# Kernel optimization log

Measured on AMD Instinct MI355X. Metric: run time of the kernel, lower is better.

Reference implementation:

```python
import jax, jax.numpy as jnp
import numpy as np

NUM_HEADS = 8
EMBED_CH = 512   # k channels
OUT_CH = 256     # v channels
MASK_CURRENT = False
NEG_INF = -1e30


def setup_inputs() -> dict:
    key = jax.random.key(0)
    ks = jax.random.split(key, 7)
    N, C, H, W = 8, 256, 32, 32
    s = lambda fan: 1.0 / np.sqrt(fan)
    return {
        "x": jax.random.normal(ks[0], (N, C, H, W), jnp.float32),
        "Wq": jax.random.normal(ks[1], (EMBED_CH, C), jnp.float32) * s(C),
        "bq": jax.random.normal(ks[2], (EMBED_CH,), jnp.float32) * 0.01,
        "Wkv": jax.random.normal(ks[3], (EMBED_CH + OUT_CH, C), jnp.float32) * s(C),
        "bkv": jax.random.normal(ks[4], (EMBED_CH + OUT_CH,), jnp.float32) * 0.01,
        "Wo": jax.random.normal(ks[5], (OUT_CH, OUT_CH), jnp.float32) * s(OUT_CH),
        "bo": jax.random.normal(ks[6], (OUT_CH,), jnp.float32) * 0.01,
    }


def _to_multihead(t, n, T):
    # t: [n, h*d, T] with channel layout '(h d)' -> [n, h, T, d]
    h = NUM_HEADS
    return t.reshape(n, h, -1, T).transpose(0, 1, 3, 2)


def reference(x, Wq, bq, Wkv, bkv, Wo, bo):
    n, C, H, W = x.shape
    T = H * W
    xf = x.reshape(n, C, T)  # flatten spatial dims into sequence

    # 1x1 convs == pointwise channel GEMMs
    q = jnp.einsum('oc,nct->not', Wq, xf) + bq[None, :, None]
    kv = jnp.einsum('oc,nct->not', Wkv, xf) + bkv[None, :, None]
    k, v = kv[:, :EMBED_CH], kv[:, EMBED_CH:]

    q = _to_multihead(q, n, T)   # [n, h, T, dk]
    k = _to_multihead(k, n, T)   # [n, h, T, dk]
    v = _to_multihead(v, n, T)   # [n, h, T, dv]

    dk = k.shape[-1]
    scale = 1.0 / np.sqrt(dk).astype(np.float32)

    # causal mask over flattened spatial positions (lower-triangular)
    diag = -1 if MASK_CURRENT else 0
    mask = jnp.tril(jnp.ones((T, T), dtype=bool), k=diag)  # [T, T]

    attn = jnp.einsum('nhtd,nhsd->nhts', q, k) * scale
    attn = jnp.where(mask[None, None], attn, NEG_INF)
    attn = jax.nn.softmax(attn, axis=-1)
    attn = jnp.where(mask[None, None], attn, 0.0)

    out = jnp.einsum('nhts,nhsd->nhtd', attn, v)            # [n, h, T, dv]
    out = out.transpose(0, 1, 3, 2).reshape(n, OUT_CH, T)   # n (h d) t

    out = jnp.einsum('oc,nct->not', Wo, out) + bo[None, :, None]
    return out.reshape(n, OUT_CH, H, W)
```

## Files before the change

### kernel.cpp

```cpp
#include <hip/hip_runtime.h>
#include <hip/hip_bf16.h>
#include <math.h>

typedef __bf16 bf16;
typedef __attribute__((ext_vector_type(4))) __bf16 bf16x4;
typedef __attribute__((ext_vector_type(8))) __bf16 bf16x8;
typedef __attribute__((ext_vector_type(4))) float f32x4;

#define T_DIM 1024
#define C_DIM 256
#define HEADS 8

static __device__ __forceinline__ int tb(int row, int col) {
  return row * 128 + ((((col >> 3) ^ row) & 7) << 4) + ((col & 7) << 1);
}

static __device__ __forceinline__ void gl16(const char* g, char* l) {
  __builtin_amdgcn_global_load_lds(
      (const __attribute__((address_space(1))) unsigned int*)g,
      (__attribute__((address_space(3))) unsigned int*)l, 16, 0, 0);
}
static __device__ __forceinline__ void stage16k(const char* g, char* l, int tid) {
  const int w = (tid >> 6) * 1024, ln = (tid & 63) * 16;
#pragma unroll
  for (int i = 0; i < 4; ++i) gl16(g + i * 4096 + w + ln, l + i * 4096 + w);
}
static __device__ __forceinline__ void stage8k(const char* g, char* l, int tid) {
  const int w = (tid >> 6) * 1024, ln = (tid & 63) * 16;
#pragma unroll
  for (int i = 0; i < 2; ++i) gl16(g + i * 4096 + w + ln, l + i * 4096 + w);
}
static __device__ __forceinline__ void stage4k(const char* g, char* l, int tid) {
  gl16(g + (tid >> 6) * 1024 + (tid & 63) * 16, l + (tid >> 6) * 1024);
}

__global__ __launch_bounds__(256) void k_prep(const float* __restrict__ x,
    const float* __restrict__ Wq, const float* __restrict__ Wkv, const float* __restrict__ Wo,
    char* __restrict__ xTt, char* __restrict__ Wbt, char* __restrict__ Wot) {
  const int tid = threadIdx.x;
  const int b = blockIdx.x;
  if (b < 512) {
    __shared__ float tile[64][65];
    const int n = b >> 6, rem = b & 63, tt64 = rem >> 2, ct = (rem & 3) << 6;
    const float* xp = x + ((size_t)n * C_DIM + ct) * T_DIM + tt64 * 64;
    const int t = tid & 63, c0 = tid >> 6;
#pragma unroll
    for (int i = 0; i < 16; ++i) tile[c0 + i * 4][t] = xp[(size_t)(c0 + i * 4) * T_DIM + t];
    __syncthreads();
    char* dst = xTt + (((size_t)(n * 8 + (tt64 >> 1))) * 4 + (rem & 3)) * 16384;
    const int rbase = (tt64 & 1) * 64;
#pragma unroll
    for (int i = 0; i < 2; ++i) {
      const int idx = tid + i * 256;
      const int tl = idx >> 3, c8 = (idx & 7) * 8;
      bf16x8 v;
#pragma unroll
      for (int j = 0; j < 8; ++j) v[j] = (bf16)tile[c8 + j][tl];
      *(bf16x8*)(dst + tb(rbase + tl, c8)) = v;
    }
  } else {
    const bool isWo = (b >= 532);
    const int o0 = (b - (isWo ? 532 : 512)) * 64;
#pragma unroll
    for (int i = 0; i < 8; ++i) {
      const int idx = tid + i * 256;
      const int row = idx >> 5, c8 = (idx & 31) * 8;
      const int o = o0 + row;
      const float* src = isWo ? (Wo + (size_t)o * C_DIM + c8)
                              : (o < 512 ? Wq + (size_t)o * C_DIM + c8
                                         : Wkv + (size_t)(o - 512) * C_DIM + c8);
      float4 a = *(const float4*)src;
      float4 bq4 = *(const float4*)(src + 4);
      bf16x8 v;
      v[0]=(bf16)a.x; v[1]=(bf16)a.y; v[2]=(bf16)a.z; v[3]=(bf16)a.w;
      v[4]=(bf16)bq4.x; v[5]=(bf16)bq4.y; v[6]=(bf16)bq4.z; v[7]=(bf16)bq4.w;
      char* base = isWo ? Wot : Wbt;
      char* dst = base + (((size_t)(o >> 7)) * 4 + (c8 >> 6)) * 16384;
      *(bf16x8*)(dst + tb(o & 127, c8 & 63)) = v;
    }
  }
}

__global__ __launch_bounds__(256) void k_qkv(const char* __restrict__ Wbt, const char* __restrict__ xTt,
    const float* __restrict__ bq, const float* __restrict__ bkv,
    bf16* __restrict__ q_ws, char* __restrict__ Kt, char* __restrict__ Vt) {
  __shared__ __attribute__((aligned(128))) unsigned char smem[32768];
  const int tid = threadIdx.x;
  const int nt = blockIdx.x, mt = blockIdx.y, n = blockIdx.z;
  const int w = tid >> 6, lane = tid & 63, lrow = lane & 15, lg = lane >> 4;
  const int wm = (w >> 1) * 64, wn = (w & 1) * 64;
  const char* gA = Wbt + (size_t)mt * 65536;
  const char* gB = xTt + ((size_t)(n * 8 + nt)) * 65536;

  f32x4 acc[4][4] = {};
#pragma unroll 1
  for (int kk = 0; kk < 4; ++kk) {
    stage16k(gA + kk * 16384, (char*)smem, tid);
    stage16k(gB + kk * 16384, (char*)smem + 16384, tid);
    __syncthreads();
    const char* As = (const char*)smem;
    const char* Bs = As + 16384;
    bf16x8 af[4][2], bv[4][2];
#pragma unroll
    for (int mi = 0; mi < 4; ++mi)
#pragma unroll
      for (int kh = 0; kh < 2; ++kh)
        af[mi][kh] = *(const bf16x8*)(As + tb(wm + mi * 16 + lrow, kh * 32 + lg * 8));
#pragma unroll
    for (int ni = 0; ni < 4; ++ni)
#pragma unroll
      for (int kh = 0; kh < 2; ++kh)
        bv[ni][kh] = *(const bf16x8*)(Bs + tb(wn + ni * 16 + lrow, kh * 32 + lg * 8));
#pragma unroll
    for (int kh = 0; kh < 2; ++kh)
#pragma unroll
      for (int mi = 0; mi < 4; ++mi)
#pragma unroll
        for (int ni = 0; ni < 4; ++ni)
          acc[mi][ni] = __builtin_amdgcn_mfma_f32_16x16x32_bf16(af[mi][kh], bv[ni][kh], acc[mi][ni], 0, 0, 0);
    __syncthreads();
  }

  const int obase = mt * 128 + wm + lg * 4;
  const int tcol0 = nt * 128 + wn + lrow;
#pragma unroll
  for (int mi = 0; mi < 4; ++mi) {
    const int o = obase + mi * 16;
    if (mt < 4) {
      const float4 bb = *(const float4*)(bq + o);
      const int nh = n * 8 + (o >> 6), d = o & 63;
      bf16* qrow = q_ws + (size_t)nh * (T_DIM * 64) + d;
#pragma unroll
      for (int ni = 0; ni < 4; ++ni) {
        const int t = tcol0 + ni * 16;
        f32x4 v = acc[mi][ni];
        bf16x4 pk;
        pk[0]=(bf16)(v[0]+bb.x); pk[1]=(bf16)(v[1]+bb.y); pk[2]=(bf16)(v[2]+bb.z); pk[3]=(bf16)(v[3]+bb.w);
        *(bf16x4*)(qrow + (size_t)t * 64) = pk;
      }
    } else if (mt < 8) {
      const int o2 = o - 512;
      const float4 bb = *(const float4*)(bkv + o2);
      const int nh = n * 8 + (o2 >> 6), d = o2 & 63;
      char* tbase = Kt + (size_t)nh * 16 * 8192;
#pragma unroll
      for (int ni = 0; ni < 4; ++ni) {
        const int t = tcol0 + ni * 16;
        f32x4 v = acc[mi][ni];
        bf16x4 pk;
        pk[0]=(bf16)(v[0]+bb.x); pk[1]=(bf16)(v[1]+bb.y); pk[2]=(bf16)(v[2]+bb.z); pk[3]=(bf16)(v[3]+bb.w);
        *(bf16x4*)(tbase + (t >> 6) * 8192 + tb(t & 63, d)) = pk;
      }
    } else {
      const int o3 = o - 1024;
      const float4 bb = *(const float4*)(bkv + 512 + o3);
      const float* bbp = (const float*)&bb;
      const int nh = n * 8 + (o3 >> 5), dv = o3 & 31;
      char* tbase = Vt + (size_t)nh * 16 * 4096;
#pragma unroll
      for (int ni = 0; ni < 4; ++ni) {
        const int t = tcol0 + ni * 16;
        f32x4 v = acc[mi][ni];
        char* tile = tbase + (t >> 6) * 4096;
#pragma unroll
        for (int r = 0; r < 4; ++r)
          *(bf16*)(tile + tb(dv + r, t & 63)) = (bf16)(v[r] + bbp[r]);
      }
    }
  }
}

__global__ __launch_bounds__(256) void k_attn(const bf16* __restrict__ q_ws,
    const char* __restrict__ Kt, const char* __restrict__ Vt, char* __restrict__ attTt) {
  __shared__ __attribute__((aligned(128))) unsigned char smem[20480];
  const int tid = threadIdx.x;
  const int nh = blockIdx.x, qp = blockIdx.y;
  const int w = tid >> 6, lane = tid & 63, lrow = lane & 15, lg = lane >> 4;

  const char* Ktb = Kt + (size_t)nh * 16 * 8192;
  const char* Vtb = Vt + (size_t)nh * 16 * 4096;
  const char* Kb = (const char*)smem;
  const char* Vb = (const char*)smem + 8192;
  char* pw = (char*)smem + 12288 + w * 2048;
  const int n = nh >> 3, h = nh & 7;
  const float s2 = 0.18033688f;

#pragma unroll 1
  for (int ph = 0; ph < 2; ++ph) {
    const int qt = ph ? (15 - qp) : qp;
    const int tg = qt * 64 + w * 16 + lrow;
    const bf16* qbase = q_ws + ((size_t)nh * T_DIM + tg) * 64;
    const bf16x8 qf0 = *(const bf16x8*)(qbase + lg * 8);
    const bf16x8 qf1 = *(const bf16x8*)(qbase + 32 + lg * 8);

    float m = -INFINITY, l = 0.f;
    f32x4 oacc[2] = {};

    for (int st = 0; st <= qt; ++st) {
      stage8k(Ktb + st * 8192, (char*)smem, tid);
      stage4k(Vtb + st * 4096, (char*)smem + 8192, tid);
      __syncthreads();

      f32x4 sacc[4];
#pragma unroll
      for (int rt = 0; rt < 4; ++rt) {
        f32x4 a = {0.f, 0.f, 0.f, 0.f};
        bf16x8 kf0 = *(const bf16x8*)(Kb + tb(rt * 16 + lrow, lg * 8));
        a = __builtin_amdgcn_mfma_f32_16x16x32_bf16(kf0, qf0, a, 0, 0, 0);
        bf16x8 kf1 = *(const bf16x8*)(Kb + tb(rt * 16 + lrow, 32 + lg * 8));
        a = __builtin_amdgcn_mfma_f32_16x16x32_bf16(kf1, qf1, a, 0, 0, 0);
        sacc[rt] = a;
      }

      float p[16];
      const bool diag = (st == qt);
      const int tl = w * 16 + lrow;
#pragma unroll
      for (int rt = 0; rt < 4; ++rt)
#pragma unroll
        for (int r = 0; r < 4; ++r) {
          float v = sacc[rt][r] * s2;
          if (diag && (rt * 16 + lg * 4 + r) > tl) v = -INFINITY;
          p[rt * 4 + r] = v;
        }

      float pmax = p[0];
#pragma unroll
      for (int i = 1; i < 16; ++i) pmax = fmaxf(pmax, p[i]);
      pmax = fmaxf(pmax, __shfl_xor(pmax, 16));
      pmax = fmaxf(pmax, __shfl_xor(pmax, 32));
      const float mn = fmaxf(m, pmax);
      const float corr = exp2f(m - mn);
      float ps = 0.f;
#pragma unroll
      for (int i = 0; i < 16; ++i) { p[i] = exp2f(p[i] - mn); ps += p[i]; }
      ps += __shfl_xor(ps, 16);
      ps += __shfl_xor(ps, 32);
      l = l * corr + ps;
      m = mn;
      oacc[0] = oacc[0] * corr;
      oacc[1] = oacc[1] * corr;

#pragma unroll
      for (int rt = 0; rt < 4; ++rt) {
        bf16x4 pk;
#pragma unroll
        for (int r = 0; r < 4; ++r) pk[r] = (bf16)p[rt * 4 + r];
        *(bf16x4*)(pw + tb(lrow, rt * 16 + lg * 4)) = pk;
      }

#pragma unroll
      for (int ks = 0; ks < 2; ++ks) {
        bf16x8 pf = *(const bf16x8*)(pw + tb(lrow, ks * 32 + lg * 8));
#pragma unroll
        for (int dt = 0; dt < 2; ++dt) {
          bf16x8 vf = *(const bf16x8*)(Vb + tb(dt * 16 + lrow, ks * 32 + lg * 8));
          oacc[dt] = __builtin_amdgcn_mfma_f32_16x16x32_bf16(vf, pf, oacc[dt], 0, 0, 0);
        }
      }
      __syncthreads();
    }

    const float inv = 1.0f / l;
    const int ntt = tg >> 7, row = tg & 127;
#pragma unroll
    for (int dt = 0; dt < 2; ++dt) {
      const int c = h * 32 + dt * 16 + lg * 4;
      char* tile = attTt + (((size_t)(n * 8 + ntt)) * 4 + (c >> 6)) * 16384;
      bf16x4 pk;
#pragma unroll
      for (int r = 0; r < 4; ++r) pk[r] = (bf16)(oacc[dt][r] * inv);
      *(bf16x4*)(tile + tb(row, c & 63)) = pk;
    }
  }
}

__global__ __launch_bounds__(256) void k_proj(const char* __restrict__ attTt,
    const char* __restrict__ Wot, const float* __restrict__ bo, float* __restrict__ out) {
  __shared__ __attribute__((aligned(128))) unsigned char smem[24576];
  const int tid = threadIdx.x;
  const int tm = blockIdx.x, om = blockIdx.y, n = blockIdx.z;
  const int w = tid >> 6, lane = tid & 63, lrow = lane & 15, lg = lane >> 4;
  const int wm = (w >> 1) * 64, wn = (w & 1) * 32;
  const char* gA = attTt + ((size_t)(n * 8 + tm)) * 65536;
  const char* gB = Wot + (size_t)(om >> 1) * 65536 + (om & 1) * 8192;

  f32x4 acc[4][2] = {};
#pragma unroll 1
  for (int kk = 0; kk < 4; ++kk) {
    stage16k(gA + kk * 16384, (char*)smem, tid);
    stage8k(gB + kk * 16384, (char*)smem + 16384, tid);
    __syncthreads();
    const char* As = (const char*)smem;
    const char* Bs = As + 16384;
    bf16x8 af[4][2], bv[2][2];
#pragma unroll
    for (int mi = 0; mi < 4; ++mi)
#pragma unroll
      for (int kh = 0; kh < 2; ++kh)
        af[mi][kh] = *(const bf16x8*)(As + tb(wm + mi * 16 + lrow, kh * 32 + lg * 8));
#pragma unroll
    for (int ni = 0; ni < 2; ++ni)
#pragma unroll
      for (int kh = 0; kh < 2; ++kh)
        bv[ni][kh] = *(const bf16x8*)(Bs + tb(wn + ni * 16 + lrow, kh * 32 + lg * 8));
#pragma unroll
    for (int kh = 0; kh < 2; ++kh)
#pragma unroll
      for (int mi = 0; mi < 4; ++mi)
#pragma unroll
        for (int ni = 0; ni < 2; ++ni)
          acc[mi][ni] = __builtin_amdgcn_mfma_f32_16x16x32_bf16(af[mi][kh], bv[ni][kh], acc[mi][ni], 0, 0, 0);
    __syncthreads();
  }

  const int t0b = tm * 128 + wm + lg * 4;
  const int ob = om * 64 + wn + lrow;
#pragma unroll
  for (int mi = 0; mi < 4; ++mi) {
    const int t0 = t0b + mi * 16;
#pragma unroll
    for (int ni = 0; ni < 2; ++ni) {
      const int o = ob + ni * 16;
      const float bb = bo[o];
      f32x4 v = acc[mi][ni];
      v[0] += bb; v[1] += bb; v[2] += bb; v[3] += bb;
      *(f32x4*)(out + ((size_t)(n * C_DIM + o)) * T_DIM + t0) = v;
    }
  }
}

extern "C" void kernel_launch(void* const* d_in, const int* in_sizes, int n_in,
                              void* d_out, int out_size, void* d_ws, size_t ws_size,
                              hipStream_t stream) {
  const float* x   = (const float*)d_in[0];
  const float* Wq  = (const float*)d_in[1];
  const float* bq  = (const float*)d_in[2];
  const float* Wkv = (const float*)d_in[3];
  const float* bkv = (const float*)d_in[4];
  const float* Wo  = (const float*)d_in[5];
  const float* bo  = (const float*)d_in[6];
  float* out = (float*)d_out;

  char* ws = (char*)d_ws;
  char* xTt   = ws;
  char* Wbt   = ws + (4u  << 20);
  char* Wot   = ws + (5u  << 20);
  bf16* q_ws  = (bf16*)(ws + (6u << 20));
  char* Kt    = ws + (14u << 20);
  char* Vt    = ws + (22u << 20);
  char* attTt = ws + (26u << 20);

  k_prep<<<536, 256, 0, stream>>>(x, Wq, Wkv, Wo, xTt, Wbt, Wot);
  k_qkv<<<dim3(8, 10, 8), 256, 0, stream>>>(Wbt, xTt, bq, bkv, q_ws, Kt, Vt);
  k_attn<<<dim3(64, 8), 256, 0, stream>>>(q_ws, Kt, Vt, attTt);
  k_proj<<<dim3(8, 4, 8), 256, 0, stream>>>(attTt, Wot, bo, out);
}
```

Before: 60.59 us.

## Process two KV tiles per attention iteration and stage V epilogue through LDS

```diff
diff --git a/kernel.cpp b/kernel.cpp
--- a/kernel.cpp
+++ b/kernel.cpp
@@ -84,7 +84,7 @@
 __global__ __launch_bounds__(256) void k_qkv(const char* __restrict__ Wbt, const char* __restrict__ xTt,
     const float* __restrict__ bq, const float* __restrict__ bkv,
     bf16* __restrict__ q_ws, char* __restrict__ Kt, char* __restrict__ Vt) {
-  __shared__ __attribute__((aligned(128))) unsigned char smem[32768];
+  __shared__ __attribute__((aligned(128))) unsigned char smem[34816];
   const int tid = threadIdx.x;
   const int nt = blockIdx.x, mt = blockIdx.y, n = blockIdx.z;
   const int w = tid >> 6, lane = tid & 63, lrow = lane & 15, lg = lane >> 4;
@@ -123,72 +123,92 @@
 
   const int obase = mt * 128 + wm + lg * 4;
   const int tcol0 = nt * 128 + wn + lrow;
-#pragma unroll
-  for (int mi = 0; mi < 4; ++mi) {
-    const int o = obase + mi * 16;
-    if (mt < 4) {
-      const float4 bb = *(const float4*)(bq + o);
-      const int nh = n * 8 + (o >> 6), d = o & 63;
-      bf16* qrow = q_ws + (size_t)nh * (T_DIM * 64) + d;
+  if (mt < 8) {
+#pragma unroll
+    for (int mi = 0; mi < 4; ++mi) {
+      const int o = obase + mi * 16;
+      if (mt < 4) {
+        const float4 bb = *(const float4*)(bq + o);
+        const int nh = n * 8 + (o >> 6), d = o & 63;
+        bf16* qrow = q_ws + (size_t)nh * (T_DIM * 64) + d;
+#pragma unroll
+        for (int ni = 0; ni < 4; ++ni) {
+          const int t = tcol0 + ni * 16;
+          f32x4 v = acc[mi][ni];
+          bf16x4 pk;
+          pk[0]=(bf16)(v[0]+bb.x); pk[1]=(bf16)(v[1]+bb.y); pk[2]=(bf16)(v[2]+bb.z); pk[3]=(bf16)(v[3]+bb.w);
+          *(bf16x4*)(qrow + (size_t)t * 64) = pk;
+        }
+      } else {
+        const int o2 = o - 512;
+        const float4 bb = *(const float4*)(bkv + o2);
+        const int nh = n * 8 + (o2 >> 6), d = o2 & 63;
+        char* tbase = Kt + (size_t)nh * 16 * 8192;
+#pragma unroll
+        for (int ni = 0; ni < 4; ++ni) {
+          const int t = tcol0 + ni * 16;
+          f32x4 v = acc[mi][ni];
+          bf16x4 pk;
+          pk[0]=(bf16)(v[0]+bb.x); pk[1]=(bf16)(v[1]+bb.y); pk[2]=(bf16)(v[2]+bb.z); pk[3]=(bf16)(v[3]+bb.w);
+          *(bf16x4*)(tbase + (t >> 6) * 8192 + tb(t & 63, d)) = pk;
+        }
+      }
+    }
+  } else {
+    bf16* tp = (bf16*)smem;
+#pragma unroll
+    for (int mi = 0; mi < 4; ++mi) {
+      const int o3g = (mt - 8) * 128 + wm + mi * 16 + lg * 4;
+      const float4 bb = *(const float4*)(bkv + 512 + o3g);
+      const float* bbp = (const float*)&bb;
+      const int o3l = wm + mi * 16 + lg * 4;
 #pragma unroll
       for (int ni = 0; ni < 4; ++ni) {
-        const int t = tcol0 + ni * 16;
+        const int tl = wn + ni * 16 + lrow;
         f32x4 v = acc[mi][ni];
-        bf16x4 pk;
-        pk[0]=(bf16)(v[0]+bb.x); pk[1]=(bf16)(v[1]+bb.y); pk[2]=(bf16)(v[2]+bb.z); pk[3]=(bf16)(v[3]+bb.w);
-        *(bf16x4*)(qrow + (size_t)t * 64) = pk;
-      }
-    } else if (mt < 8) {
-      const int o2 = o - 512;
-      const float4 bb = *(const float4*)(bkv + o2);
-      const int nh = n * 8 + (o2 >> 6), d = o2 & 63;
-      char* tbase = Kt + (size_t)nh * 16 * 8192;
-#pragma unroll
-      for (int ni = 0; ni < 4; ++ni) {
-        const int t = tcol0 + ni * 16;
-        f32x4 v = acc[mi][ni];
-        bf16x4 pk;
-        pk[0]=(bf16)(v[0]+bb.x); pk[1]=(bf16)(v[1]+bb.y); pk[2]=(bf16)(v[2]+bb.z); pk[3]=(bf16)(v[3]+bb.w);
-        *(bf16x4*)(tbase + (t >> 6) * 8192 + tb(t & 63, d)) = pk;
-      }
-    } else {
-      const int o3 = o - 1024;
-      const float4 bb = *(const float4*)(bkv + 512 + o3);
-      const float* bbp = (const float*)&bb;
-      const int nh = n * 8 + (o3 >> 5), dv = o3 & 31;
-      char* tbase = Vt + (size_t)nh * 16 * 4096;
-#pragma unroll
-      for (int ni = 0; ni < 4; ++ni) {
-        const int t = tcol0 + ni * 16;
-        f32x4 v = acc[mi][ni];
-        char* tile = tbase + (t >> 6) * 4096;
 #pragma unroll
         for (int r = 0; r < 4; ++r)
-          *(bf16*)(tile + tb(dv + r, t & 63)) = (bf16)(v[r] + bbp[r]);
-      }
+          tp[(o3l + r) * 132 + tl] = (bf16)(v[r] + bbp[r]);
+      }
+    }
+    __syncthreads();
+    const int row = tid >> 1, half = tid & 1;
+    const int o3 = (mt - 8) * 128 + row;
+    const int nh = n * 8 + (o3 >> 5), dv = o3 & 31;
+    char* tile = Vt + (size_t)nh * 16 * 4096 + (nt * 2 + half) * 4096;
+    const bf16* src = tp + row * 132 + half * 64;
+#pragma unroll
+    for (int g = 0; g < 8; ++g) {
+      bf16x4 lo = *(const bf16x4*)(src + g * 8);
+      bf16x4 hi = *(const bf16x4*)(src + g * 8 + 4);
+      bf16x8 vv;
+      vv[0]=lo[0]; vv[1]=lo[1]; vv[2]=lo[2]; vv[3]=lo[3];
+      vv[4]=hi[0]; vv[5]=hi[1]; vv[6]=hi[2]; vv[7]=hi[3];
+      *(bf16x8*)(tile + tb(dv, g * 8)) = vv;
     }
   }
 }
 
 __global__ __launch_bounds__(256) void k_attn(const bf16* __restrict__ q_ws,
     const char* __restrict__ Kt, const char* __restrict__ Vt, char* __restrict__ attTt) {
-  __shared__ __attribute__((aligned(128))) unsigned char smem[20480];
+  __shared__ __attribute__((aligned(128))) unsigned char smem[40960];
   const int tid = threadIdx.x;
   const int nh = blockIdx.x, qp = blockIdx.y;
   const int w = tid >> 6, lane = tid & 63, lrow = lane & 15, lg = lane >> 4;
 
   const char* Ktb = Kt + (size_t)nh * 16 * 8192;
   const char* Vtb = Vt + (size_t)nh * 16 * 4096;
-  const char* Kb = (const char*)smem;
-  const char* Vb = (const char*)smem + 8192;
-  char* pw = (char*)smem + 12288 + w * 2048;
+  char* Kb[2] = { (char*)smem, (char*)smem + 8192 };
+  char* Vb[2] = { (char*)smem + 16384, (char*)smem + 20480 };
+  char* pw[2] = { (char*)smem + 24576 + w * 4096, (char*)smem + 24576 + w * 4096 + 2048 };
   const int n = nh >> 3, h = nh & 7;
   const float s2 = 0.18033688f;
+  const int tl = w * 16 + lrow;
 
 #pragma unroll 1
   for (int ph = 0; ph < 2; ++ph) {
     const int qt = ph ? (15 - qp) : qp;
-    const int tg = qt * 64 + w * 16 + lrow;
+    const int tg = qt * 64 + tl;
     const bf16* qbase = q_ws + ((size_t)nh * T_DIM + tg) * 64;
     const bf16x8 qf0 = *(const bf16x8*)(qbase + lg * 8);
     const bf16x8 qf1 = *(const bf16x8*)(qbase + 32 + lg * 8);
@@ -196,31 +216,107 @@
     float m = -INFINITY, l = 0.f;
     f32x4 oacc[2] = {};
 
-    for (int st = 0; st <= qt; ++st) {
-      stage8k(Ktb + st * 8192, (char*)smem, tid);
-      stage4k(Vtb + st * 4096, (char*)smem + 8192, tid);
+    int st2 = 0;
+#pragma unroll 1
+    for (; st2 + 1 <= qt; st2 += 2) {
+      stage8k(Ktb + (size_t)st2 * 8192, Kb[0], tid);
+      stage8k(Ktb + (size_t)(st2 + 1) * 8192, Kb[1], tid);
+      stage4k(Vtb + (size_t)st2 * 4096, Vb[0], tid);
+      stage4k(Vtb + (size_t)(st2 + 1) * 4096, Vb[1], tid);
+      __syncthreads();
+
+      f32x4 sacc[2][4];
+#pragma unroll
+      for (int sub = 0; sub < 2; ++sub)
+#pragma unroll
+        for (int rt = 0; rt < 4; ++rt) {
+          f32x4 a = {0.f, 0.f, 0.f, 0.f};
+          bf16x8 kf0 = *(const bf16x8*)(Kb[sub] + tb(rt * 16 + lrow, lg * 8));
+          a = __builtin_amdgcn_mfma_f32_16x16x32_bf16(kf0, qf0, a, 0, 0, 0);
+          bf16x8 kf1 = *(const bf16x8*)(Kb[sub] + tb(rt * 16 + lrow, 32 + lg * 8));
+          a = __builtin_amdgcn_mfma_f32_16x16x32_bf16(kf1, qf1, a, 0, 0, 0);
+          sacc[sub][rt] = a;
+        }
+
+      const bool diag1 = (st2 + 1 == qt);
+      float p[2][16];
+#pragma unroll
+      for (int sub = 0; sub < 2; ++sub)
+#pragma unroll
+        for (int rt = 0; rt < 4; ++rt)
+#pragma unroll
+          for (int r = 0; r < 4; ++r) {
+            float v = sacc[sub][rt][r] * s2;
+            if (sub == 1 && diag1 && (rt * 16 + lg * 4 + r) > tl) v = -INFINITY;
+            p[sub][rt * 4 + r] = v;
+          }
+
+      float pmax = p[0][0];
+#pragma unroll
+      for (int i = 1; i < 16; ++i) pmax = fmaxf(pmax, p[0][i]);
+#pragma unroll
+      for (int i = 0; i < 16; ++i) pmax = fmaxf(pmax, p[1][i]);
+      pmax = fmaxf(pmax, __shfl_xor(pmax, 16));
+      pmax = fmaxf(pmax, __shfl_xor(pmax, 32));
+      const float mn = fmaxf(m, pmax);
+      const float corr = exp2f(m - mn);
+      float ps = 0.f;
+#pragma unroll
+      for (int sub = 0; sub < 2; ++sub)
+#pragma unroll
+        for (int i = 0; i < 16; ++i) { p[sub][i] = exp2f(p[sub][i] - mn); ps += p[sub][i]; }
+      ps += __shfl_xor(ps, 16);
+      ps += __shfl_xor(ps, 32);
+      l = l * corr + ps;
+      m = mn;
+      oacc[0] = oacc[0] * corr;
+      oacc[1] = oacc[1] * corr;
+
+#pragma unroll
+      for (int sub = 0; sub < 2; ++sub) {
+#pragma unroll
+        for (int rt = 0; rt < 4; ++rt) {
+          bf16x4 pk;
+#pragma unroll
+          for (int r = 0; r < 4; ++r) pk[r] = (bf16)p[sub][rt * 4 + r];
+          *(bf16x4*)(pw[sub] + tb(lrow, rt * 16 + lg * 4)) = pk;
+        }
+#pragma unroll
+        for (int ks = 0; ks < 2; ++ks) {
+          bf16x8 pf = *(const bf16x8*)(pw[sub] + tb(lrow, ks * 32 + lg * 8));
+#pragma unroll
+          for (int dt = 0; dt < 2; ++dt) {
+            bf16x8 vf = *(const bf16x8*)(Vb[sub] + tb(dt * 16 + lrow, ks * 32 + lg * 8));
+            oacc[dt] = __builtin_amdgcn_mfma_f32_16x16x32_bf16(vf, pf, oacc[dt], 0, 0, 0);
+          }
+        }
+      }
+      __syncthreads();
+    }
+
+    if (st2 <= qt) {
+      stage8k(Ktb + (size_t)st2 * 8192, Kb[0], tid);
+      stage4k(Vtb + (size_t)st2 * 4096, Vb[0], tid);
       __syncthreads();
 
       f32x4 sacc[4];
 #pragma unroll
       for (int rt = 0; rt < 4; ++rt) {
         f32x4 a = {0.f, 0.f, 0.f, 0.f};
-        bf16x8 kf0 = *(const bf16x8*)(Kb + tb(rt * 16 + lrow, lg * 8));
+        bf16x8 kf0 = *(const bf16x8*)(Kb[0] + tb(rt * 16 + lrow, lg * 8));
         a = __builtin_amdgcn_mfma_f32_16x16x32_bf16(kf0, qf0, a, 0, 0, 0);
-        bf16x8 kf1 = *(const bf16x8*)(Kb + tb(rt * 16 + lrow, 32 + lg * 8));
+        bf16x8 kf1 = *(const bf16x8*)(Kb[0] + tb(rt * 16 + lrow, 32 + lg * 8));
         a = __builtin_amdgcn_mfma_f32_16x16x32_bf16(kf1, qf1, a, 0, 0, 0);
         sacc[rt] = a;
       }
 
       float p[16];
-      const bool diag = (st == qt);
-      const int tl = w * 16 + lrow;
 #pragma unroll
       for (int rt = 0; rt < 4; ++rt)
 #pragma unroll
         for (int r = 0; r < 4; ++r) {
           float v = sacc[rt][r] * s2;
-          if (diag && (rt * 16 + lg * 4 + r) > tl) v = -INFINITY;
+          if ((rt * 16 + lg * 4 + r) > tl) v = -INFINITY;
           p[rt * 4 + r] = v;
         }
 
@@ -246,15 +342,14 @@
         bf16x4 pk;
 #pragma unroll
         for (int r = 0; r < 4; ++r) pk[r] = (bf16)p[rt * 4 + r];
-        *(bf16x4*)(pw + tb(lrow, rt * 16 + lg * 4)) = pk;
-      }
-
+        *(bf16x4*)(pw[0] + tb(lrow, rt * 16 + lg * 4)) = pk;
+      }
 #pragma unroll
       for (int ks = 0; ks < 2; ++ks) {
-        bf16x8 pf = *(const bf16x8*)(pw + tb(lrow, ks * 32 + lg * 8));
+        bf16x8 pf = *(const bf16x8*)(pw[0] + tb(lrow, ks * 32 + lg * 8));
 #pragma unroll
         for (int dt = 0; dt < 2; ++dt) {
-          bf16x8 vf = *(const bf16x8*)(Vb + tb(dt * 16 + lrow, ks * 32 + lg * 8));
+          bf16x8 vf = *(const bf16x8*)(Vb[0] + tb(dt * 16 + lrow, ks * 32 + lg * 8));
           oacc[dt] = __builtin_amdgcn_mfma_f32_16x16x32_bf16(vf, pf, oacc[dt], 0, 0, 0);
         }
       }
```

New measurement: 59.99 us. About the same (-1.0%).
